# Kernel tuning notes

Measured on AMD Instinct MI355X. Metric: run time of the kernel, lower is better.

The kernel has to match this reference:

```python
import jax, jax.numpy as jnp
from jax import lax
import numpy as np

B, T, D = 64, 1024, 512
H = D // 2  # per-direction LSTM hidden size; concat fwd+bwd -> D


def _lstm_dir(x_tbd, W_ih, W_hh, b):
    # x_tbd: [T, B, D]; torch gate order i, f, g, o
    Bd = x_tbd.shape[1]
    Hd = W_hh.shape[1]

    def step(carry, x_t):
        h, c = carry
        g = x_t @ W_ih.T + h @ W_hh.T + b  # [B, 4H]
        i, f, gg, o = jnp.split(g, 4, axis=-1)
        c = jax.nn.sigmoid(f) * c + jax.nn.sigmoid(i) * jnp.tanh(gg)
        h = jax.nn.sigmoid(o) * jnp.tanh(c)
        return (h, c), h

    init = (jnp.zeros((Bd, Hd), x_tbd.dtype), jnp.zeros((Bd, Hd), x_tbd.dtype))
    _, hs = lax.scan(step, init, x_tbd)
    return hs  # [T, B, H]


def setup_inputs() -> dict:
    key = jax.random.key(0)
    ks = jax.random.split(key, 10)
    s_ih = 1.0 / np.sqrt(D)
    s_hh = 1.0 / np.sqrt(H)
    inp = {
        "x": jax.random.normal(ks[0], (B, T, D), jnp.float32),
        "W_ih_f": jax.random.uniform(ks[1], (4 * H, D), jnp.float32, -s_ih, s_ih),
        "W_hh_f": jax.random.uniform(ks[2], (4 * H, H), jnp.float32, -s_hh, s_hh),
        "b_f": jax.random.uniform(ks[3], (4 * H,), jnp.float32, -s_hh, s_hh),
        "W_ih_b": jax.random.uniform(ks[4], (4 * H, D), jnp.float32, -s_ih, s_ih),
        "W_hh_b": jax.random.uniform(ks[5], (4 * H, H), jnp.float32, -s_hh, s_hh),
        "b_b": jax.random.uniform(ks[6], (4 * H,), jnp.float32, -s_hh, s_hh),
        "lin_w": jax.random.normal(ks[7], (1, D), jnp.float32) * (1.0 / np.sqrt(D)),
        "lin_b": jnp.zeros((1,), jnp.float32),
        "ln_g": jnp.ones((D,), jnp.float32),
        "ln_b": jnp.zeros((D,), jnp.float32),
        "mask": jnp.ones((B, 1, T), dtype=bool),
        "input_len": T,
        "k": 20,
    }
    return inp


def reference(x, W_ih_f, W_hh_f, b_f, W_ih_b, W_hh_b, b_b, lin_w, lin_b,
              ln_g, ln_b, mask, input_len, k):
    x_tbd = jnp.transpose(x, (1, 0, 2))  # [T, B, D]
    h_f = _lstm_dir(x_tbd, W_ih_f, W_hh_f, b_f)                      # [T, B, H]
    h_b = _lstm_dir(x_tbd[::-1], W_ih_b, W_hh_b, b_b)[::-1]          # [T, B, H]
    lstm_o = jnp.transpose(jnp.concatenate([h_f, h_b], axis=-1), (1, 0, 2))  # [B, T, D]

    # linear -> squeeze -> softmax over seq dim
    logits = (lstm_o @ lin_w.T).squeeze(-1) + lin_b[0]  # [B, T]
    list_out = jax.nn.softmax(logits, axis=-1)

    # topk smallest (largest=False)
    _, indices = lax.top_k(-list_out, k)  # [B, k]

    # layer norm (eps=1e-5)
    mu = jnp.mean(lstm_o, axis=-1, keepdims=True)
    var = jnp.mean(jnp.square(lstm_o - mu), axis=-1, keepdims=True)
    lstm_o_n = (lstm_o - mu) * lax.rsqrt(var + 1e-5) * ln_g + ln_b

    # vectorized per-batch column scatter: mask[b, :, indices[b]] = False
    hit = jnp.zeros((B, T), dtype=bool).at[jnp.arange(B)[:, None], indices].set(True)
    sgn_mask = mask & ~hit[:, None, :]  # [B, 1, T]

    return (indices, lstm_o_n, sgn_mask)
```

## Files before the change

### kernel.cpp

```cpp
#include <hip/hip_runtime.h>
#include <math.h>

#define Bz 64
#define Tz 1024
#define Dz 512
#define Hz 256
#define Gz 1024
#define Kz 20

__device__ __forceinline__ float sigf(float x) { return 1.0f / (1.0f + __expf(-x)); }

__global__ __launch_bounds__(256) void init_ws(int* p) {
    int i = blockIdx.x * 256 + threadIdx.x;
    if (i < 100352) p[i] = 0;
}

__global__ __launch_bounds__(256) void gates_gemm(
    const float* __restrict__ x,
    const float* __restrict__ Wf, const float* __restrict__ Wb,
    const float* __restrict__ bf, const float* __restrict__ bb,
    float* __restrict__ G, int Tc, int base)
{
    __shared__ __align__(16) float As[16][68];
    __shared__ __align__(16) float Bs[16][68];
    const int tid   = threadIdx.x;
    const int mtile = blockIdx.x;
    const int sl    = blockIdx.y;
    const int dir   = blockIdx.z;

    const float* W    = dir ? Wb : Wf;
    const float* bias = dir ? bb : bf;
    const int s = base + sl;
    const int t = dir ? (Tz - 1 - s) : s;

    const int lr = tid >> 2;
    const int lk = (tid & 3) * 4;
    const float* Arow = W + (size_t)(mtile * 64 + lr) * Dz;
    const float* Brow = x + ((size_t)lr * Tz + t) * Dz;

    const int mg = tid >> 4;
    const int ng = tid & 15;
    float acc[4][4] = {};

    for (int kt = 0; kt < Dz; kt += 16) {
        float4 a4 = *(const float4*)(Arow + kt + lk);
        float4 b4 = *(const float4*)(Brow + kt + lk);
        __syncthreads();
        As[lk + 0][lr] = a4.x; As[lk + 1][lr] = a4.y;
        As[lk + 2][lr] = a4.z; As[lk + 3][lr] = a4.w;
        Bs[lk + 0][lr] = b4.x; Bs[lk + 1][lr] = b4.y;
        Bs[lk + 2][lr] = b4.z; Bs[lk + 3][lr] = b4.w;
        __syncthreads();
#pragma unroll
        for (int kk = 0; kk < 16; ++kk) {
            float4 av = *(const float4*)&As[kk][mg * 4];
            float4 bv = *(const float4*)&Bs[kk][ng * 4];
            acc[0][0] = fmaf(av.x, bv.x, acc[0][0]);
            acc[0][1] = fmaf(av.x, bv.y, acc[0][1]);
            acc[0][2] = fmaf(av.x, bv.z, acc[0][2]);
            acc[0][3] = fmaf(av.x, bv.w, acc[0][3]);
            acc[1][0] = fmaf(av.y, bv.x, acc[1][0]);
            acc[1][1] = fmaf(av.y, bv.y, acc[1][1]);
            acc[1][2] = fmaf(av.y, bv.z, acc[1][2]);
            acc[1][3] = fmaf(av.y, bv.w, acc[1][3]);
            acc[2][0] = fmaf(av.z, bv.x, acc[2][0]);
            acc[2][1] = fmaf(av.z, bv.y, acc[2][1]);
            acc[2][2] = fmaf(av.z, bv.z, acc[2][2]);
            acc[2][3] = fmaf(av.z, bv.w, acc[2][3]);
            acc[3][0] = fmaf(av.w, bv.x, acc[3][0]);
            acc[3][1] = fmaf(av.w, bv.y, acc[3][1]);
            acc[3][2] = fmaf(av.w, bv.z, acc[3][2]);
            acc[3][3] = fmaf(av.w, bv.w, acc[3][3]);
        }
    }
#pragma unroll
    for (int i = 0; i < 4; ++i) {
        int row = mtile * 64 + mg * 4 + i;
        float bvs = bias[row];
        float4 o;
        o.x = acc[i][0] + bvs; o.y = acc[i][1] + bvs;
        o.z = acc[i][2] + bvs; o.w = acc[i][3] + bvs;
        *(float4*)(G + (((size_t)dir * Gz + row) * Tc + sl) * 64 + ng * 4) = o;
    }
}

__global__ __launch_bounds__(512, 1) void lstm_rec(
    const float* __restrict__ G,
    const float* __restrict__ Whf, const float* __restrict__ Whb,
    float* __restrict__ hbuf,
    float* __restrict__ cbuf,
    float* __restrict__ out1,
    int* pflag, int Tc, int base)
{
    __shared__ __align__(16) float h_l[Hz * 64 + 512];
    __shared__ __align__(16) float part_l[4][16][64];

    const int tid = threadIdx.x;
    const int dir = blockIdx.x >> 6;
    const int g   = blockIdx.x & 63;
    const float* __restrict__ Whh = dir ? Whb : Whf;

    const int b    = tid & 63;
    const int w_id = __builtin_amdgcn_readfirstlane(tid >> 6);
    const int kq   = w_id & 3;
    const int rh   = w_id >> 2;

    const float* Wr[8];
#pragma unroll
    for (int i = 0; i < 8; ++i) {
        int rl = rh * 8 + i;
        int q = rl >> 2, j = rl & 3;
        Wr[i] = Whh + (size_t)(q * Hz + g * 4 + j) * Hz + kq * 64;
    }

    const int j_ = tid >> 6;
    float c_reg = 0.0f;
    if (tid < 256) c_reg = cbuf[((size_t)dir * Hz + g * 4 + j_) * 64 + b];

    for (int sl = 0; sl < Tc; ++sl) {
        const int s = base + sl;

        float gpre[4];
        if (tid < 256) {
#pragma unroll
            for (int q = 0; q < 4; ++q)
                gpre[q] = G[(((size_t)dir * Gz + q * Hz + g * 4 + j_) * Tc + sl) * 64 + b];
        }

        if (s > 0) {
            if (tid < 64) {
                const int* fp = pflag + dir * 64 + tid;
                for (;;) {
                    int v = __hip_atomic_load(fp, __ATOMIC_RELAXED,
                                              __HIP_MEMORY_SCOPE_AGENT);
                    if (__all(v >= s)) break;
                    __builtin_amdgcn_s_sleep(2);
                }
            }
            __syncthreads();
        }

        const unsigned long long* hsrc = (const unsigned long long*)
            (hbuf + (size_t)((s & 1) * 2 + dir) * Hz * 64);
        unsigned long long tmp[16];
#pragma unroll
        for (int jj = 0; jj < 16; ++jj)
            tmp[jj] = __hip_atomic_load(hsrc + jj * 512 + tid,
                                        __ATOMIC_RELAXED, __HIP_MEMORY_SCOPE_AGENT);
#pragma unroll
        for (int jj = 0; jj < 16; ++jj)
            ((unsigned long long*)h_l)[jj * 512 + tid] = tmp[jj];
        __syncthreads();

        float acc[8] = {};
        const float* hb = h_l + (size_t)(kq * 64) * 64 + b;
#pragma unroll 4
        for (int k = 0; k < 64; k += 4) {
            const float h0 = hb[(k + 0) * 64];
            const float h1 = hb[(k + 1) * 64];
            const float h2 = hb[(k + 2) * 64];
            const float h3 = hb[(k + 3) * 64];
#pragma unroll
            for (int i = 0; i < 8; ++i) {
                const float4 wv = *(const float4*)(Wr[i] + k);
                acc[i] = fmaf(h3, wv.w, fmaf(h2, wv.z,
                         fmaf(h1, wv.y, fmaf(h0, wv.x, acc[i]))));
            }
        }
#pragma unroll
        for (int i = 0; i < 8; ++i) part_l[kq][rh * 8 + i][b] = acc[i];
        __syncthreads();

        float hv = 0.0f;
        if (tid < 256) {
            float gv[4];
#pragma unroll
            for (int q = 0; q < 4; ++q) {
                const int rl = q * 4 + j_;
                gv[q] = gpre[q] + part_l[0][rl][b] + part_l[1][rl][b]
                      + part_l[2][rl][b] + part_l[3][rl][b];
            }
            const float gi = sigf(gv[0]);
            const float gf = sigf(gv[1]);
            const float gg = tanhf(gv[2]);
            const float go = sigf(gv[3]);
            c_reg = gf * c_reg + gi * gg;
            hv = go * tanhf(c_reg);
            const int hx = g * 4 + j_;
            __hip_atomic_store(
                hbuf + ((size_t)(((s + 1) & 1) * 2 + dir) * Hz + hx) * 64 + b, hv,
                __ATOMIC_RELAXED, __HIP_MEMORY_SCOPE_AGENT);
        }

        asm volatile("s_waitcnt vmcnt(0)" ::: "memory");
        __syncthreads();
        if (tid == 0)
            __hip_atomic_store(pflag + dir * 64 + g, s + 1,
                               __ATOMIC_RELAXED, __HIP_MEMORY_SCOPE_AGENT);

        if (tid < 256) {
            const int tt = dir ? (Tz - 1 - s) : s;
            out1[((size_t)b * Tz + tt) * Dz + dir * Hz + g * 4 + j_] = hv;
        }
    }
    if (tid < 256) cbuf[((size_t)dir * Hz + g * 4 + j_) * 64 + b] = c_reg;
}

__global__ __launch_bounds__(256) void head_kernel(
    const float* __restrict__ out1, const float* __restrict__ lin_w,
    const float* __restrict__ lin_b, const unsigned char* __restrict__ mask8,
    float* __restrict__ out0, float* __restrict__ out2)
{
    __shared__ __align__(16) float lw[Dz];
    __shared__ float llog[Tz];
    __shared__ unsigned char hit[Tz];
    __shared__ float redv[4];
    __shared__ int   redi[4];

    const int tid = threadIdx.x;
    const int bb  = blockIdx.x;
    for (int i = tid; i < Dz; i += 256) lw[i] = lin_w[i];
    for (int i = tid; i < Tz; i += 256) hit[i] = 0;
    __syncthreads();

    const int w = tid >> 6, lane = tid & 63;
    const float lbv = lin_b[0];
    for (int t = w; t < Tz; t += 4) {
        const float* rp = out1 + ((size_t)bb * Tz + t) * Dz + lane * 8;
        float4 a0 = *(const float4*)rp;
        float4 a1 = *(const float4*)(rp + 4);
        const float* wp = lw + lane * 8;
        float ps = a0.x * wp[0] + a0.y * wp[1] + a0.z * wp[2] + a0.w * wp[3]
                 + a1.x * wp[4] + a1.y * wp[5] + a1.z * wp[6] + a1.w * wp[7];
        for (int o = 32; o; o >>= 1) ps += __shfl_down(ps, o);
        if (lane == 0) llog[t] = ps + lbv;
    }
    __syncthreads();

    for (int it = 0; it < Kz; ++it) {
        float bv = 3.4e38f; int bi = Tz - 1;
        for (int t = tid; t < Tz; t += 256) {
            float v = llog[t];
            if (v < bv) { bv = v; bi = t; }
        }
        for (int o = 32; o; o >>= 1) {
            float ov = __shfl_down(bv, o);
            int   oi = __shfl_down(bi, o);
            if (ov < bv || (ov == bv && oi < bi)) { bv = ov; bi = oi; }
        }
        if (lane == 0) { redv[w] = bv; redi[w] = bi; }
        __syncthreads();
        if (tid == 0) {
            for (int qq = 1; qq < 4; ++qq)
                if (redv[qq] < bv || (redv[qq] == bv && redi[qq] < bi)) { bv = redv[qq]; bi = redi[qq]; }
            out0[bb * Kz + it] = (float)bi;
            llog[bi] = 3.4e38f;
            hit[bi] = 1;
        }
        __syncthreads();
    }
    for (int t = tid; t < Tz; t += 256) {
        bool mv = mask8[(size_t)bb * Tz + t] != 0;
        out2[(size_t)bb * Tz + t] = (mv && !hit[t]) ? 1.0f : 0.0f;
    }
}

__global__ __launch_bounds__(256) void ln_kernel(
    float* __restrict__ out1, const float* __restrict__ ln_g,
    const float* __restrict__ ln_b)
{
    const int tid = threadIdx.x;
    const int w = tid >> 6, lane = tid & 63;
    const size_t row = (size_t)blockIdx.x * 4 + w;
    float* rp = out1 + row * Dz + lane * 8;
    float4 a0 = *(float4*)rp;
    float4 a1 = *(float4*)(rp + 4);
    float s  = a0.x + a0.y + a0.z + a0.w + a1.x + a1.y + a1.z + a1.w;
    float sq = a0.x*a0.x + a0.y*a0.y + a0.z*a0.z + a0.w*a0.w
             + a1.x*a1.x + a1.y*a1.y + a1.z*a1.z + a1.w*a1.w;
    for (int o = 32; o; o >>= 1) { s += __shfl_down(s, o); sq += __shfl_down(sq, o); }
    s  = __shfl(s, 0);
    sq = __shfl(sq, 0);
    const float mu  = s * (1.0f / Dz);
    const float var = sq * (1.0f / Dz) - mu * mu;
    const float rs  = rsqrtf(var + 1e-5f);
    const float* gp = ln_g + lane * 8;
    const float* bp = ln_b + lane * 8;
    a0.x = (a0.x - mu) * rs * gp[0] + bp[0];
    a0.y = (a0.y - mu) * rs * gp[1] + bp[1];
    a0.z = (a0.z - mu) * rs * gp[2] + bp[2];
    a0.w = (a0.w - mu) * rs * gp[3] + bp[3];
    a1.x = (a1.x - mu) * rs * gp[4] + bp[4];
    a1.y = (a1.y - mu) * rs * gp[5] + bp[5];
    a1.z = (a1.z - mu) * rs * gp[6] + bp[6];
    a1.w = (a1.w - mu) * rs * gp[7] + bp[7];
    *(float4*)rp = a0;
    *(float4*)(rp + 4) = a1;
}

extern "C" void kernel_launch(void* const* d_in, const int* in_sizes, int n_in,
                              void* d_out, int out_size, void* d_ws, size_t ws_size,
                              hipStream_t stream)
{
    (void)in_sizes; (void)n_in; (void)out_size;
    const float* x     = (const float*)d_in[0];
    const float* Wif   = (const float*)d_in[1];
    const float* Whf   = (const float*)d_in[2];
    const float* bf    = (const float*)d_in[3];
    const float* Wib   = (const float*)d_in[4];
    const float* Whb   = (const float*)d_in[5];
    const float* bb    = (const float*)d_in[6];
    const float* lin_w = (const float*)d_in[7];
    const float* lin_b = (const float*)d_in[8];
    const float* ln_g  = (const float*)d_in[9];
    const float* ln_b  = (const float*)d_in[10];
    const unsigned char* mask8 = (const unsigned char*)d_in[11];

    float* ws    = (float*)d_ws;
    int*   flags = (int*)d_ws;
    float* hbuf  = ws + 2048;
    float* cbuf  = ws + 2048 + 65536;
    float* gates = ws + 2048 + 65536 + 32768;

    const size_t fixedBytes = (size_t)(2048 + 65536 + 32768) * 4;
    const size_t avail = ws_size > fixedBytes ? ws_size - fixedBytes : 0;
    int Tc = 8;
    for (int cand = 1024; cand >= 8; cand >>= 1) {
        if ((size_t)cand * (2ull * Gz * 64 * 4) <= avail) { Tc = cand; break; }
    }

    float* out0 = (float*)d_out;
    float* out1 = out0 + (size_t)Bz * Kz;
    float* out2 = out1 + (size_t)Bz * Tz * Dz;

    init_ws<<<dim3((100352 + 255) / 256), 256, 0, stream>>>((int*)d_ws);

    const int nChunks = Tz / Tc;
    for (int c = 0; c < nChunks; ++c) {
        const int base = c * Tc;
        gates_gemm<<<dim3(16, Tc, 2), 256, 0, stream>>>(x, Wif, Wib, bf, bb, gates, Tc, base);
        lstm_rec<<<dim3(128), 512, 0, stream>>>(gates, Whf, Whb, hbuf, cbuf, out1, flags, Tc, base);
    }
    head_kernel<<<dim3(Bz), 256, 0, stream>>>(out1, lin_w, lin_b, mask8, out0, out2);
    ln_kernel<<<dim3((Bz * Tz) / 4), 256, 0, stream>>>(out1, ln_g, ln_b);
}
```

Baseline: 12.51 ms.

## Repartition LSTM recurrence by batch slices with register-resident weights and stamped exchange

The recurrent kernel is reorganized so each of 256 blocks owns a 2-sample batch slice and a quarter of the hidden dimension. Its slice of W_hh is held in registers, which removes the per-step weight reload. Partial gate sums go to the other three quarter-blocks through a global buffer of stamped 64-bit value+step pairs. Each block polls those stamps, so the global per-step flag barrier and the full h broadcast through global memory are gone. The costs are much higher register pressure (128 weight floats per thread), a larger zeroed workspace, and a requirement that all 256 blocks be co-resident to avoid deadlock.

```diff
diff --git a/kernel.cpp b/kernel.cpp
--- a/kernel.cpp
+++ b/kernel.cpp
@@ -7,12 +7,19 @@
 #define Hz 256
 #define Gz 1024
 #define Kz 20
+#define NBS 32
+
+#define WS_ZERO_DWORDS (2097152 + 32768 + 32768)
 
 __device__ __forceinline__ float sigf(float x) { return 1.0f / (1.0f + __expf(-x)); }
+
+__device__ __forceinline__ unsigned long long packsv(float v, unsigned st) {
+    return ((unsigned long long)st << 32) | (unsigned long long)__float_as_uint(v);
+}
 
 __global__ __launch_bounds__(256) void init_ws(int* p) {
     int i = blockIdx.x * 256 + threadIdx.x;
-    if (i < 100352) p[i] = 0;
+    if (i < WS_ZERO_DWORDS) p[i] = 0;
 }
 
 __global__ __launch_bounds__(256) void gates_gemm(
@@ -87,123 +94,152 @@
 __global__ __launch_bounds__(512, 1) void lstm_rec(
     const float* __restrict__ G,
     const float* __restrict__ Whf, const float* __restrict__ Whb,
-    float* __restrict__ hbuf,
-    float* __restrict__ cbuf,
+    unsigned long long* __restrict__ xbuf,
+    float* __restrict__ hstate,
+    float* __restrict__ cstate,
     float* __restrict__ out1,
-    int* pflag, int Tc, int base)
-{
-    __shared__ __align__(16) float h_l[Hz * 64 + 512];
-    __shared__ __align__(16) float part_l[4][16][64];
+    int Tc, int base)
+{
+    __shared__ __align__(16) float h_l[64][2];
+    __shared__ __align__(16) float selfP[256][2];
+    __shared__ __align__(16) float gl[256][2];
 
     const int tid = threadIdx.x;
-    const int dir = blockIdx.x >> 6;
-    const int g   = blockIdx.x & 63;
+    const int blk = blockIdx.x;
+    const int dir = blk >> 7;
+    const int kq  = (blk >> 5) & 3;
+    const int bs  = blk & 31;
     const float* __restrict__ Whh = dir ? Whb : Whf;
 
-    const int b    = tid & 63;
-    const int w_id = __builtin_amdgcn_readfirstlane(tid >> 6);
-    const int kq   = w_id & 3;
-    const int rh   = w_id >> 2;
-
-    const float* Wr[8];
-#pragma unroll
-    for (int i = 0; i < 8; ++i) {
-        int rl = rh * 8 + i;
-        int q = rl >> 2, j = rl & 3;
-        Wr[i] = Whh + (size_t)(q * Hz + g * 4 + j) * Hz + kq * 64;
-    }
-
-    const int j_ = tid >> 6;
+    const int r0 = tid * 2;
+    float w0[64], w1[64];
+    {
+        const float* p0 = Whh + (size_t)r0 * Hz + kq * 64;
+        const float* p1 = p0 + Hz;
+#pragma unroll
+        for (int i = 0; i < 16; ++i) {
+            float4 a = *(const float4*)(p0 + 4 * i);
+            float4 c = *(const float4*)(p1 + 4 * i);
+            w0[4*i+0] = a.x; w0[4*i+1] = a.y; w0[4*i+2] = a.z; w0[4*i+3] = a.w;
+            w1[4*i+0] = c.x; w1[4*i+1] = c.y; w1[4*i+2] = c.z; w1[4*i+3] = c.w;
+        }
+    }
+    const int dst  = (tid >> 5) & 3;
+    const int rowp = (r0 >> 8) * 64 + (r0 & 63);
+
+    const int arow = tid >> 1;
+    const int ab   = tid & 1;
+    const int growA = (arow >> 6) * 256 + kq * 64 + (arow & 63);
+    const int bglo  = bs * 2;
+
+    int srcs[3];
+    { int n = 0; for (int ss = 0; ss < 4; ++ss) if (ss != kq) srcs[n++] = ss; }
+
+    size_t ob[2], ib[2];
+#pragma unroll
+    for (int p = 0; p < 2; ++p) {
+        ob[p] = (((((size_t)p*2 + dir)*NBS + bs)*4 + dst)*4 + kq)*512 + (size_t)rowp*2;
+        ib[p] = ((((size_t)p*2 + dir)*NBS + bs)*4 + kq)*4*512 + (size_t)arow*2 + ab;
+    }
+
     float c_reg = 0.0f;
-    if (tid < 256) c_reg = cbuf[((size_t)dir * Hz + g * 4 + j_) * 64 + b];
+    {
+        const size_t sb = ((size_t)(dir * NBS + bs) * 4 + kq) * 128;
+        if (tid < 128) {
+            h_l[tid >> 1][tid & 1] = hstate[sb + tid];
+            c_reg = cstate[sb + tid];
+        }
+    }
+    __syncthreads();
 
     for (int sl = 0; sl < Tc; ++sl) {
         const int s = base + sl;
-
-        float gpre[4];
-        if (tid < 256) {
-#pragma unroll
-            for (int q = 0; q < 4; ++q)
-                gpre[q] = G[(((size_t)dir * Gz + q * Hz + g * 4 + j_) * Tc + sl) * 64 + b];
-        }
-
-        if (s > 0) {
-            if (tid < 64) {
-                const int* fp = pflag + dir * 64 + tid;
-                for (;;) {
-                    int v = __hip_atomic_load(fp, __ATOMIC_RELAXED,
-                                              __HIP_MEMORY_SCOPE_AGENT);
-                    if (__all(v >= s)) break;
-                    __builtin_amdgcn_s_sleep(2);
-                }
+        const unsigned stamp = (unsigned)(s + 1);
+        const int par = s & 1;
+
+        const float gval =
+            G[(((size_t)dir * Gz + growA) * Tc + sl) * 64 + (bglo + ab)];
+
+        float a00 = 0.f, a01 = 0.f, a10 = 0.f, a11 = 0.f;
+#pragma unroll
+        for (int kk = 0; kk < 64; kk += 2) {
+            const float4 hv = *(const float4*)(&h_l[kk][0]);
+            a00 = fmaf(w0[kk],     hv.x, a00);
+            a01 = fmaf(w0[kk],     hv.y, a01);
+            a10 = fmaf(w1[kk],     hv.x, a10);
+            a11 = fmaf(w1[kk],     hv.y, a11);
+            a00 = fmaf(w0[kk + 1], hv.z, a00);
+            a01 = fmaf(w0[kk + 1], hv.w, a01);
+            a10 = fmaf(w1[kk + 1], hv.z, a10);
+            a11 = fmaf(w1[kk + 1], hv.w, a11);
+        }
+
+        if (dst == kq) {
+            *(float4*)&selfP[rowp][0] = make_float4(a00, a01, a10, a11);
+        } else {
+            unsigned long long* op = xbuf + ob[par];
+            __hip_atomic_store(op + 0, packsv(a00, stamp),
+                               __ATOMIC_RELAXED, __HIP_MEMORY_SCOPE_AGENT);
+            __hip_atomic_store(op + 1, packsv(a01, stamp),
+                               __ATOMIC_RELAXED, __HIP_MEMORY_SCOPE_AGENT);
+            __hip_atomic_store(op + 2, packsv(a10, stamp),
+                               __ATOMIC_RELAXED, __HIP_MEMORY_SCOPE_AGENT);
+            __hip_atomic_store(op + 3, packsv(a11, stamp),
+                               __ATOMIC_RELAXED, __HIP_MEMORY_SCOPE_AGENT);
+        }
+        __syncthreads();
+
+        {
+            const unsigned long long* ibp = xbuf + ib[par];
+            const unsigned long long* i0 = ibp + (size_t)srcs[0] * 512;
+            const unsigned long long* i1 = ibp + (size_t)srcs[1] * 512;
+            const unsigned long long* i2 = ibp + (size_t)srcs[2] * 512;
+            unsigned long long v0 = __hip_atomic_load(i0, __ATOMIC_RELAXED,
+                                                      __HIP_MEMORY_SCOPE_AGENT);
+            unsigned long long v1 = __hip_atomic_load(i1, __ATOMIC_RELAXED,
+                                                      __HIP_MEMORY_SCOPE_AGENT);
+            unsigned long long v2 = __hip_atomic_load(i2, __ATOMIC_RELAXED,
+                                                      __HIP_MEMORY_SCOPE_AGENT);
+            for (;;) {
+                const bool o0 = (unsigned)(v0 >> 32) == stamp;
+                const bool o1 = (unsigned)(v1 >> 32) == stamp;
+                const bool o2 = (unsigned)(v2 >> 32) == stamp;
+                if (o0 & o1 & o2) break;
+                __builtin_amdgcn_s_sleep(1);
+                if (!o0) v0 = __hip_atomic_load(i0, __ATOMIC_RELAXED,
+                                                __HIP_MEMORY_SCOPE_AGENT);
+                if (!o1) v1 = __hip_atomic_load(i1, __ATOMIC_RELAXED,
+                                                __HIP_MEMORY_SCOPE_AGENT);
+                if (!o2) v2 = __hip_atomic_load(i2, __ATOMIC_RELAXED,
+                                                __HIP_MEMORY_SCOPE_AGENT);
             }
-            __syncthreads();
-        }
-
-        const unsigned long long* hsrc = (const unsigned long long*)
-            (hbuf + (size_t)((s & 1) * 2 + dir) * Hz * 64);
-        unsigned long long tmp[16];
-#pragma unroll
-        for (int jj = 0; jj < 16; ++jj)
-            tmp[jj] = __hip_atomic_load(hsrc + jj * 512 + tid,
-                                        __ATOMIC_RELAXED, __HIP_MEMORY_SCOPE_AGENT);
-#pragma unroll
-        for (int jj = 0; jj < 16; ++jj)
-            ((unsigned long long*)h_l)[jj * 512 + tid] = tmp[jj];
-        __syncthreads();
-
-        float acc[8] = {};
-        const float* hb = h_l + (size_t)(kq * 64) * 64 + b;
-#pragma unroll 4
-        for (int k = 0; k < 64; k += 4) {
-            const float h0 = hb[(k + 0) * 64];
-            const float h1 = hb[(k + 1) * 64];
-            const float h2 = hb[(k + 2) * 64];
-            const float h3 = hb[(k + 3) * 64];
-#pragma unroll
-            for (int i = 0; i < 8; ++i) {
-                const float4 wv = *(const float4*)(Wr[i] + k);
-                acc[i] = fmaf(h3, wv.w, fmaf(h2, wv.z,
-                         fmaf(h1, wv.y, fmaf(h0, wv.x, acc[i]))));
-            }
-        }
-#pragma unroll
-        for (int i = 0; i < 8; ++i) part_l[kq][rh * 8 + i][b] = acc[i];
-        __syncthreads();
-
-        float hv = 0.0f;
-        if (tid < 256) {
-            float gv[4];
-#pragma unroll
-            for (int q = 0; q < 4; ++q) {
-                const int rl = q * 4 + j_;
-                gv[q] = gpre[q] + part_l[0][rl][b] + part_l[1][rl][b]
-                      + part_l[2][rl][b] + part_l[3][rl][b];
-            }
-            const float gi = sigf(gv[0]);
-            const float gf = sigf(gv[1]);
-            const float gg = tanhf(gv[2]);
-            const float go = sigf(gv[3]);
+            gl[arow][ab] = gval + selfP[arow][ab]
+                         + __uint_as_float((unsigned)v0)
+                         + __uint_as_float((unsigned)v1)
+                         + __uint_as_float((unsigned)v2);
+        }
+        __syncthreads();
+
+        if (tid < 128) {
+            const int bj = tid >> 1, bb2 = tid & 1;
+            const float gi = sigf(gl[bj][bb2]);
+            const float gf = sigf(gl[64 + bj][bb2]);
+            const float gg = tanhf(gl[128 + bj][bb2]);
+            const float go = sigf(gl[192 + bj][bb2]);
             c_reg = gf * c_reg + gi * gg;
-            hv = go * tanhf(c_reg);
-            const int hx = g * 4 + j_;
-            __hip_atomic_store(
-                hbuf + ((size_t)(((s + 1) & 1) * 2 + dir) * Hz + hx) * 64 + b, hv,
-                __ATOMIC_RELAXED, __HIP_MEMORY_SCOPE_AGENT);
-        }
-
-        asm volatile("s_waitcnt vmcnt(0)" ::: "memory");
-        __syncthreads();
-        if (tid == 0)
-            __hip_atomic_store(pflag + dir * 64 + g, s + 1,
-                               __ATOMIC_RELAXED, __HIP_MEMORY_SCOPE_AGENT);
-
-        if (tid < 256) {
+            const float hv = go * tanhf(c_reg);
+            h_l[bj][bb2] = hv;
             const int tt = dir ? (Tz - 1 - s) : s;
-            out1[((size_t)b * Tz + tt) * Dz + dir * Hz + g * 4 + j_] = hv;
-        }
-    }
-    if (tid < 256) cbuf[((size_t)dir * Hz + g * 4 + j_) * 64 + b] = c_reg;
+            out1[((size_t)(bglo + bb2) * Tz + tt) * Dz + dir * Hz + kq * 64 + bj] = hv;
+        }
+        __syncthreads();
+    }
+
+    if (tid < 128) {
+        const size_t sb = ((size_t)(dir * NBS + bs) * 4 + kq) * 128;
+        hstate[sb + tid] = h_l[tid >> 1][tid & 1];
+        cstate[sb + tid] = c_reg;
+    }
 }
 
 __global__ __launch_bounds__(256) void head_kernel(
@@ -316,13 +352,13 @@
     const float* ln_b  = (const float*)d_in[10];
     const unsigned char* mask8 = (const unsigned char*)d_in[11];
 
-    float* ws    = (float*)d_ws;
-    int*   flags = (int*)d_ws;
-    float* hbuf  = ws + 2048;
-    float* cbuf  = ws + 2048 + 65536;
-    float* gates = ws + 2048 + 65536 + 32768;
-
-    const size_t fixedBytes = (size_t)(2048 + 65536 + 32768) * 4;
+    float* ws = (float*)d_ws;
+    unsigned long long* xbuf = (unsigned long long*)ws;
+    float* hstate = ws + 2097152;
+    float* cstate = hstate + 32768;
+    float* gates  = cstate + 32768;
+
+    const size_t fixedBytes = (size_t)(2097152 + 65536) * 4;
     const size_t avail = ws_size > fixedBytes ? ws_size - fixedBytes : 0;
     int Tc = 8;
     for (int cand = 1024; cand >= 8; cand >>= 1) {
@@ -333,13 +369,14 @@
     float* out1 = out0 + (size_t)Bz * Kz;
     float* out2 = out1 + (size_t)Bz * Tz * Dz;
 
-    init_ws<<<dim3((100352 + 255) / 256), 256, 0, stream>>>((int*)d_ws);
+    init_ws<<<dim3((WS_ZERO_DWORDS + 255) / 256), 256, 0, stream>>>((int*)d_ws);
 
     const int nChunks = Tz / Tc;
     for (int c = 0; c < nChunks; ++c) {
         const int base = c * Tc;
         gates_gemm<<<dim3(16, Tc, 2), 256, 0, stream>>>(x, Wif, Wib, bf, bb, gates, Tc, base);
-        lstm_rec<<<dim3(128), 512, 0, stream>>>(gates, Whf, Whb, hbuf, cbuf, out1, flags, Tc, base);
+        lstm_rec<<<dim3(256), 512, 0, stream>>>(gates, Whf, Whb, xbuf, hstate, cstate,
+                                                out1, Tc, base);
     }
     head_kernel<<<dim3(Bz), 256, 0, stream>>>(out1, lin_w, lin_b, mask8, out0, out2);
     ln_kernel<<<dim3((Bz * Tz) / 4), 256, 0, stream>>>(out1, ln_g, ln_b);
```

After: 10.51 ms. 16.0% less time.

## Fuse input-gate GEMM and recurrence into one persistent producer-consumer kernel

Applied to the files above, without the earlier changes.

Replaces the chunked gates_gemm plus lstm_rec launches with a single persistent kernel. 128 blocks run the recurrence, each owning a batch slice and a K-quarter with W_hh held in registers and partial sums exchanged through stamped global buffers. The other 128 blocks compute the input projection into an 8-slot ring and are gated by progress flags. This removes per-chunk launch overhead and the large gates buffer, and overlaps the input GEMM with the sequential recurrence. In exchange it depends on all 256 blocks being co-resident and on fine-grained spin synchronization across blocks, and the 128 registers per thread used to hold weights risk spilling.

```diff
diff --git a/kernel.cpp b/kernel.cpp
--- a/kernel.cpp
+++ b/kernel.cpp
@@ -8,202 +8,287 @@
 #define Gz 1024
 #define Kz 20
 
+#define CTRL_DW  256
+#define XBUF_U64 786432
+#define ZERO_DW  (CTRL_DW + XBUF_U64 * 2)
+#define RING_DW  (8 * 2 * 1024 * 64)
+
 __device__ __forceinline__ float sigf(float x) { return 1.0f / (1.0f + __expf(-x)); }
+
+__device__ __forceinline__ unsigned long long packsv(float v, unsigned st) {
+    return ((unsigned long long)st << 32) | (unsigned long long)__float_as_uint(v);
+}
+__device__ __forceinline__ unsigned long long pack2(float a, float b) {
+    return ((unsigned long long)__float_as_uint(b) << 32) |
+           (unsigned long long)__float_as_uint(a);
+}
 
 __global__ __launch_bounds__(256) void init_ws(int* p) {
     int i = blockIdx.x * 256 + threadIdx.x;
-    if (i < 100352) p[i] = 0;
-}
-
-__global__ __launch_bounds__(256) void gates_gemm(
+    if (i < ZERO_DW) p[i] = 0;
+}
+
+__global__ __launch_bounds__(512, 1) void fused_lstm(
     const float* __restrict__ x,
-    const float* __restrict__ Wf, const float* __restrict__ Wb,
-    const float* __restrict__ bf, const float* __restrict__ bb,
-    float* __restrict__ G, int Tc, int base)
+    const float* __restrict__ Wif, const float* __restrict__ Whf,
+    const float* __restrict__ bf,
+    const float* __restrict__ Wib, const float* __restrict__ Whb,
+    const float* __restrict__ bb,
+    float* __restrict__ out1, int* __restrict__ ctrl)
 {
-    __shared__ __align__(16) float As[16][68];
-    __shared__ __align__(16) float Bs[16][68];
-    const int tid   = threadIdx.x;
-    const int mtile = blockIdx.x;
-    const int sl    = blockIdx.y;
-    const int dir   = blockIdx.z;
-
-    const float* W    = dir ? Wb : Wf;
-    const float* bias = dir ? bb : bf;
-    const int s = base + sl;
-    const int t = dir ? (Tz - 1 - s) : s;
-
-    const int lr = tid >> 2;
-    const int lk = (tid & 3) * 4;
-    const float* Arow = W + (size_t)(mtile * 64 + lr) * Dz;
-    const float* Brow = x + ((size_t)lr * Tz + t) * Dz;
-
-    const int mg = tid >> 4;
-    const int ng = tid & 15;
-    float acc[4][4] = {};
-
-    for (int kt = 0; kt < Dz; kt += 16) {
-        float4 a4 = *(const float4*)(Arow + kt + lk);
-        float4 b4 = *(const float4*)(Brow + kt + lk);
+    __shared__ __align__(16) float smem[34880];
+    int* gcnt = ctrl;
+    int* prog = ctrl + 8;
+    unsigned long long* xbuf = (unsigned long long*)(ctrl + CTRL_DW);
+    float* Gring = (float*)(ctrl + CTRL_DW + XBUF_U64 * 2);
+
+    const int tid = threadIdx.x;
+    const int blk = blockIdx.x;
+
+    if (blk < 128) {
+        const int dir = blk >> 6;
+        const int kq  = (blk >> 4) & 3;
+        const int bs  = blk & 15;
+        const float* __restrict__ Whh = dir ? Whb : Whf;
+
+        float* h_l   = smem;
+        float* selfP = smem + 256;
+        float* gl    = smem + 1280;
+
+        const int r0 = tid * 2;
+        float w0[64], w1[64];
+        {
+            const float* p0 = Whh + (size_t)r0 * Hz + kq * 64;
+            const float* p1 = p0 + Hz;
+#pragma unroll
+            for (int i = 0; i < 16; ++i) {
+                float4 a = *(const float4*)(p0 + 4 * i);
+                float4 c = *(const float4*)(p1 + 4 * i);
+                w0[4*i+0]=a.x; w0[4*i+1]=a.y; w0[4*i+2]=a.z; w0[4*i+3]=a.w;
+                w1[4*i+0]=c.x; w1[4*i+1]=c.y; w1[4*i+2]=c.z; w1[4*i+3]=c.w;
+            }
+        }
+        const int dst  = (r0 >> 6) & 3;
+        const int rowp = (r0 >> 8) * 64 + (r0 & 63);
+        const int srci = kq - (kq > dst ? 1 : 0);
+
+        const int arow  = tid >> 1;
+        const int bp    = tid & 1;
+        const int growA = (arow >> 6) * 256 + kq * 64 + (arow & 63);
+        const int bglo  = bs * 4;
+
+        size_t ob[2], ib[2];
+#pragma unroll
+        for (int p = 0; p < 2; ++p) {
+            size_t o = ((((size_t)p * 2 + dir) * 16 + bs) * 4 + dst) * 3 + srci;
+            ob[p] = o * 1024 + (size_t)rowp * 4;
+            size_t q = ((((size_t)p * 2 + dir) * 16 + bs) * 4 + kq) * 3;
+            ib[p] = q * 1024 + (size_t)arow * 4 + 2 * bp;
+        }
+
+        for (int i = tid; i < 256; i += 512) h_l[i] = 0.0f;
+        float c_reg = 0.0f;
+        const int rr = tid >> 2, bb2 = tid & 3;
         __syncthreads();
-        As[lk + 0][lr] = a4.x; As[lk + 1][lr] = a4.y;
-        As[lk + 2][lr] = a4.z; As[lk + 3][lr] = a4.w;
-        Bs[lk + 0][lr] = b4.x; Bs[lk + 1][lr] = b4.y;
-        Bs[lk + 2][lr] = b4.z; Bs[lk + 3][lr] = b4.w;
+
+        for (int s = 0; s < Tz; ++s) {
+            const unsigned stamp = (unsigned)(s + 1);
+            const int par = s & 1;
+
+            if ((s & 1) == 0) {
+                const int sp = s >> 1;
+                const int tgt = ((sp >> 2) + 1) * 16;
+                if (tid < 64) {
+                    const int* gp = gcnt + dir * 4 + (sp & 3);
+                    while (__hip_atomic_load(gp, __ATOMIC_RELAXED,
+                                             __HIP_MEMORY_SCOPE_AGENT) < tgt)
+                        __builtin_amdgcn_s_sleep(2);
+                }
+                __syncthreads();
+            }
+
+            const unsigned long long* Gp = (const unsigned long long*)
+                (Gring + ((size_t)((s & 7) * 2 + dir) * 1024 + growA) * 64
+                       + bglo + 2 * bp);
+            unsigned long long gv = __hip_atomic_load(Gp, __ATOMIC_RELAXED,
+                                                      __HIP_MEMORY_SCOPE_AGENT);
+
+            float a0[4] = {}, a1[4] = {};
+#pragma unroll
+            for (int k = 0; k < 64; ++k) {
+                const float4 hv = *(const float4*)(h_l + k * 4);
+                const float wa = w0[k], wc = w1[k];
+                a0[0] = fmaf(wa, hv.x, a0[0]); a0[1] = fmaf(wa, hv.y, a0[1]);
+                a0[2] = fmaf(wa, hv.z, a0[2]); a0[3] = fmaf(wa, hv.w, a0[3]);
+                a1[0] = fmaf(wc, hv.x, a1[0]); a1[1] = fmaf(wc, hv.y, a1[1]);
+                a1[2] = fmaf(wc, hv.z, a1[2]); a1[3] = fmaf(wc, hv.w, a1[3]);
+            }
+
+            if (dst == kq) {
+                *(float4*)(selfP + rowp * 4)     = make_float4(a0[0],a0[1],a0[2],a0[3]);
+                *(float4*)(selfP + rowp * 4 + 4) = make_float4(a1[0],a1[1],a1[2],a1[3]);
+            } else {
+                unsigned long long* op = xbuf + ob[par];
+#pragma unroll
+                for (int j = 0; j < 4; ++j)
+                    __hip_atomic_store(op + j, packsv(a0[j], stamp),
+                                       __ATOMIC_RELAXED, __HIP_MEMORY_SCOPE_AGENT);
+#pragma unroll
+                for (int j = 0; j < 4; ++j)
+                    __hip_atomic_store(op + 4 + j, packsv(a1[j], stamp),
+                                       __ATOMIC_RELAXED, __HIP_MEMORY_SCOPE_AGENT);
+            }
+            __syncthreads();
+
+            {
+                const unsigned long long* i0 = xbuf + ib[par];
+                const unsigned long long* ps[6] =
+                    { i0, i0 + 1, i0 + 1024, i0 + 1025, i0 + 2048, i0 + 2049 };
+                unsigned long long v[6];
+#pragma unroll
+                for (int j = 0; j < 6; ++j)
+                    v[j] = __hip_atomic_load(ps[j], __ATOMIC_RELAXED,
+                                             __HIP_MEMORY_SCOPE_AGENT);
+                for (;;) {
+                    bool ok = true;
+#pragma unroll
+                    for (int j = 0; j < 6; ++j)
+                        ok &= ((unsigned)(v[j] >> 32) == stamp);
+                    if (ok) break;
+                    __builtin_amdgcn_s_sleep(1);
+#pragma unroll
+                    for (int j = 0; j < 6; ++j)
+                        if ((unsigned)(v[j] >> 32) != stamp)
+                            v[j] = __hip_atomic_load(ps[j], __ATOMIC_RELAXED,
+                                                     __HIP_MEMORY_SCOPE_AGENT);
+                }
+                gl[arow * 4 + 2 * bp] =
+                    __uint_as_float((unsigned)gv) + selfP[arow * 4 + 2 * bp]
+                    + __uint_as_float((unsigned)v[0])
+                    + __uint_as_float((unsigned)v[2])
+                    + __uint_as_float((unsigned)v[4]);
+                gl[arow * 4 + 2 * bp + 1] =
+                    __uint_as_float((unsigned)(gv >> 32)) + selfP[arow * 4 + 2 * bp + 1]
+                    + __uint_as_float((unsigned)v[1])
+                    + __uint_as_float((unsigned)v[3])
+                    + __uint_as_float((unsigned)v[5]);
+            }
+            __syncthreads();
+
+            float hv_s = 0.0f;
+            if (tid < 256) {
+                const float gi = sigf(gl[rr * 4 + bb2]);
+                const float gf = sigf(gl[(64 + rr) * 4 + bb2]);
+                const float gg = tanhf(gl[(128 + rr) * 4 + bb2]);
+                const float go = sigf(gl[(192 + rr) * 4 + bb2]);
+                c_reg = gf * c_reg + gi * gg;
+                hv_s = go * tanhf(c_reg);
+                h_l[rr * 4 + bb2] = hv_s;
+            }
+            __syncthreads();
+            if (kq == 0 && tid == 0)
+                __hip_atomic_store(prog + dir * 16 + bs, s,
+                                   __ATOMIC_RELAXED, __HIP_MEMORY_SCOPE_AGENT);
+            if (tid < 256) {
+                const int tt = dir ? (Tz - 1 - s) : s;
+                out1[((size_t)(bglo + bb2) * Tz + tt) * Dz + dir * Hz + kq * 64 + rr] = hv_s;
+            }
+        }
+    } else {
+        const int g2      = blk - 128;
+        const int rowtile = g2 & 15;
+        const int dir     = (g2 >> 4) & 1;
+        const int phase   = (g2 >> 5) & 3;
+        const float* __restrict__ Wih  = dir ? Wib : Wif;
+        const float* __restrict__ bias = dir ? bb : bf;
+
+        float* Bs  = smem;
+        float* A_l = smem + 2112;
+
+        const int mg = tid >> 5;
+        const int ng = tid & 31;
+        const float4 bias4 = *(const float4*)(bias + rowtile * 64 + mg * 4);
+
+        for (int idx = tid * 4; idx < 64 * 512; idx += 2048) {
+            const int r = idx >> 9, k = idx & 511;
+            const float4 a = *(const float4*)(Wih + (size_t)(rowtile * 64 + r) * Dz + k);
+            A_l[(k + 0) * 64 + r] = a.x; A_l[(k + 1) * 64 + r] = a.y;
+            A_l[(k + 2) * 64 + r] = a.z; A_l[(k + 3) * 64 + r] = a.w;
+        }
         __syncthreads();
-#pragma unroll
-        for (int kk = 0; kk < 16; ++kk) {
-            float4 av = *(const float4*)&As[kk][mg * 4];
-            float4 bv = *(const float4*)&Bs[kk][ng * 4];
-            acc[0][0] = fmaf(av.x, bv.x, acc[0][0]);
-            acc[0][1] = fmaf(av.x, bv.y, acc[0][1]);
-            acc[0][2] = fmaf(av.x, bv.z, acc[0][2]);
-            acc[0][3] = fmaf(av.x, bv.w, acc[0][3]);
-            acc[1][0] = fmaf(av.y, bv.x, acc[1][0]);
-            acc[1][1] = fmaf(av.y, bv.y, acc[1][1]);
-            acc[1][2] = fmaf(av.y, bv.z, acc[1][2]);
-            acc[1][3] = fmaf(av.y, bv.w, acc[1][3]);
-            acc[2][0] = fmaf(av.z, bv.x, acc[2][0]);
-            acc[2][1] = fmaf(av.z, bv.y, acc[2][1]);
-            acc[2][2] = fmaf(av.z, bv.z, acc[2][2]);
-            acc[2][3] = fmaf(av.z, bv.w, acc[2][3]);
-            acc[3][0] = fmaf(av.w, bv.x, acc[3][0]);
-            acc[3][1] = fmaf(av.w, bv.y, acc[3][1]);
-            acc[3][2] = fmaf(av.w, bv.z, acc[3][2]);
-            acc[3][3] = fmaf(av.w, bv.w, acc[3][3]);
+
+        const int nn   = tid & 127;
+        const int ko   = (tid >> 7) * 4;
+        const int bcol = nn & 63;
+        const int slx  = nn >> 6;
+        const int ssl  = ng >> 4;
+        const int bc0  = (ng & 15) * 4;
+
+        for (int sp = phase; sp < 512; sp += 4) {
+            const int s0 = 2 * sp;
+            const int ttx = dir ? (Tz - 1 - (s0 + slx)) : (s0 + slx);
+            const float* xp = x + ((size_t)bcol * Tz + ttx) * Dz;
+
+            float4 bq = *(const float4*)(xp + ko);
+            float acc[4][4] = {};
+            for (int kt = 0; kt < 512; kt += 16) {
+                __syncthreads();
+                Bs[(ko + 0) * 132 + nn] = bq.x;
+                Bs[(ko + 1) * 132 + nn] = bq.y;
+                Bs[(ko + 2) * 132 + nn] = bq.z;
+                Bs[(ko + 3) * 132 + nn] = bq.w;
+                __syncthreads();
+                if (kt + 16 < 512) bq = *(const float4*)(xp + kt + 16 + ko);
+#pragma unroll
+                for (int kk = 0; kk < 16; ++kk) {
+                    const float4 av = *(const float4*)(A_l + (kt + kk) * 64 + mg * 4);
+                    const float4 bv = *(const float4*)(Bs + kk * 132 + ng * 4);
+                    acc[0][0]=fmaf(av.x,bv.x,acc[0][0]); acc[0][1]=fmaf(av.x,bv.y,acc[0][1]);
+                    acc[0][2]=fmaf(av.x,bv.z,acc[0][2]); acc[0][3]=fmaf(av.x,bv.w,acc[0][3]);
+                    acc[1][0]=fmaf(av.y,bv.x,acc[1][0]); acc[1][1]=fmaf(av.y,bv.y,acc[1][1]);
+                    acc[1][2]=fmaf(av.y,bv.z,acc[1][2]); acc[1][3]=fmaf(av.y,bv.w,acc[1][3]);
+                    acc[2][0]=fmaf(av.z,bv.x,acc[2][0]); acc[2][1]=fmaf(av.z,bv.y,acc[2][1]);
+                    acc[2][2]=fmaf(av.z,bv.z,acc[2][2]); acc[2][3]=fmaf(av.z,bv.w,acc[2][3]);
+                    acc[3][0]=fmaf(av.w,bv.x,acc[3][0]); acc[3][1]=fmaf(av.w,bv.y,acc[3][1]);
+                    acc[3][2]=fmaf(av.w,bv.z,acc[3][2]); acc[3][3]=fmaf(av.w,bv.w,acc[3][3]);
+                }
+            }
+
+            if (sp >= 4) {
+                const int tgt = 2 * sp - 6;
+                if (tid < 64) {
+                    for (;;) {
+                        int pv = (tid < 16)
+                            ? __hip_atomic_load(prog + dir * 16 + tid,
+                                                __ATOMIC_RELAXED, __HIP_MEMORY_SCOPE_AGENT)
+                            : 0x7fffffff;
+                        if (__all(pv >= tgt)) break;
+                        __builtin_amdgcn_s_sleep(2);
+                    }
+                }
+            }
+            __syncthreads();
+
+            const int slot = (s0 + ssl) & 7;
+            float* gbase = Gring + ((size_t)(slot * 2 + dir) * 1024
+                                    + rowtile * 64 + mg * 4) * 64 + bc0;
+#pragma unroll
+            for (int i = 0; i < 4; ++i) {
+                const float bv4 = (i == 0) ? bias4.x : (i == 1) ? bias4.y
+                                 : (i == 2) ? bias4.z : bias4.w;
+                unsigned long long* gp = (unsigned long long*)(gbase + (size_t)i * 64);
+                __hip_atomic_store(gp,     pack2(acc[i][0] + bv4, acc[i][1] + bv4),
+                                   __ATOMIC_RELAXED, __HIP_MEMORY_SCOPE_AGENT);
+                __hip_atomic_store(gp + 1, pack2(acc[i][2] + bv4, acc[i][3] + bv4),
+                                   __ATOMIC_RELAXED, __HIP_MEMORY_SCOPE_AGENT);
+            }
+            asm volatile("s_waitcnt vmcnt(0)" ::: "memory");
+            __syncthreads();
+            if (tid == 0)
+                __hip_atomic_fetch_add(gcnt + dir * 4 + (sp & 3), 1,
+                                       __ATOMIC_RELAXED, __HIP_MEMORY_SCOPE_AGENT);
         }
     }
-#pragma unroll
-    for (int i = 0; i < 4; ++i) {
-        int row = mtile * 64 + mg * 4 + i;
-        float bvs = bias[row];
-        float4 o;
-        o.x = acc[i][0] + bvs; o.y = acc[i][1] + bvs;
-        o.z = acc[i][2] + bvs; o.w = acc[i][3] + bvs;
-        *(float4*)(G + (((size_t)dir * Gz + row) * Tc + sl) * 64 + ng * 4) = o;
-    }
-}
-
-__global__ __launch_bounds__(512, 1) void lstm_rec(
-    const float* __restrict__ G,
-    const float* __restrict__ Whf, const float* __restrict__ Whb,
-    float* __restrict__ hbuf,
-    float* __restrict__ cbuf,
-    float* __restrict__ out1,
-    int* pflag, int Tc, int base)
-{
-    __shared__ __align__(16) float h_l[Hz * 64 + 512];
-    __shared__ __align__(16) float part_l[4][16][64];
-
-    const int tid = threadIdx.x;
-    const int dir = blockIdx.x >> 6;
-    const int g   = blockIdx.x & 63;
-    const float* __restrict__ Whh = dir ? Whb : Whf;
-
-    const int b    = tid & 63;
-    const int w_id = __builtin_amdgcn_readfirstlane(tid >> 6);
-    const int kq   = w_id & 3;
-    const int rh   = w_id >> 2;
-
-    const float* Wr[8];
-#pragma unroll
-    for (int i = 0; i < 8; ++i) {
-        int rl = rh * 8 + i;
-        int q = rl >> 2, j = rl & 3;
-        Wr[i] = Whh + (size_t)(q * Hz + g * 4 + j) * Hz + kq * 64;
-    }
-
-    const int j_ = tid >> 6;
-    float c_reg = 0.0f;
-    if (tid < 256) c_reg = cbuf[((size_t)dir * Hz + g * 4 + j_) * 64 + b];
-
-    for (int sl = 0; sl < Tc; ++sl) {
-        const int s = base + sl;
-
-        float gpre[4];
-        if (tid < 256) {
-#pragma unroll
-            for (int q = 0; q < 4; ++q)
-                gpre[q] = G[(((size_t)dir * Gz + q * Hz + g * 4 + j_) * Tc + sl) * 64 + b];
-        }
-
-        if (s > 0) {
-            if (tid < 64) {
-                const int* fp = pflag + dir * 64 + tid;
-                for (;;) {
-                    int v = __hip_atomic_load(fp, __ATOMIC_RELAXED,
-                                              __HIP_MEMORY_SCOPE_AGENT);
-                    if (__all(v >= s)) break;
-                    __builtin_amdgcn_s_sleep(2);
-                }
-            }
-            __syncthreads();
-        }
-
-        const unsigned long long* hsrc = (const unsigned long long*)
-            (hbuf + (size_t)((s & 1) * 2 + dir) * Hz * 64);
-        unsigned long long tmp[16];
-#pragma unroll
-        for (int jj = 0; jj < 16; ++jj)
-            tmp[jj] = __hip_atomic_load(hsrc + jj * 512 + tid,
-                                        __ATOMIC_RELAXED, __HIP_MEMORY_SCOPE_AGENT);
-#pragma unroll
-        for (int jj = 0; jj < 16; ++jj)
-            ((unsigned long long*)h_l)[jj * 512 + tid] = tmp[jj];
-        __syncthreads();
-
-        float acc[8] = {};
-        const float* hb = h_l + (size_t)(kq * 64) * 64 + b;
-#pragma unroll 4
-        for (int k = 0; k < 64; k += 4) {
-            const float h0 = hb[(k + 0) * 64];
-            const float h1 = hb[(k + 1) * 64];
-            const float h2 = hb[(k + 2) * 64];
-            const float h3 = hb[(k + 3) * 64];
-#pragma unroll
-            for (int i = 0; i < 8; ++i) {
-                const float4 wv = *(const float4*)(Wr[i] + k);
-                acc[i] = fmaf(h3, wv.w, fmaf(h2, wv.z,
-                         fmaf(h1, wv.y, fmaf(h0, wv.x, acc[i]))));
-            }
-        }
-#pragma unroll
-        for (int i = 0; i < 8; ++i) part_l[kq][rh * 8 + i][b] = acc[i];
-        __syncthreads();
-
-        float hv = 0.0f;
-        if (tid < 256) {
-            float gv[4];
-#pragma unroll
-            for (int q = 0; q < 4; ++q) {
-                const int rl = q * 4 + j_;
-                gv[q] = gpre[q] + part_l[0][rl][b] + part_l[1][rl][b]
-                      + part_l[2][rl][b] + part_l[3][rl][b];
-            }
-            const float gi = sigf(gv[0]);
-            const float gf = sigf(gv[1]);
-            const float gg = tanhf(gv[2]);
-            const float go = sigf(gv[3]);
-            c_reg = gf * c_reg + gi * gg;
-            hv = go * tanhf(c_reg);
-            const int hx = g * 4 + j_;
-            __hip_atomic_store(
-                hbuf + ((size_t)(((s + 1) & 1) * 2 + dir) * Hz + hx) * 64 + b, hv,
-                __ATOMIC_RELAXED, __HIP_MEMORY_SCOPE_AGENT);
-        }
-
-        asm volatile("s_waitcnt vmcnt(0)" ::: "memory");
-        __syncthreads();
-        if (tid == 0)
-            __hip_atomic_store(pflag + dir * 64 + g, s + 1,
-                               __ATOMIC_RELAXED, __HIP_MEMORY_SCOPE_AGENT);
-
-        if (tid < 256) {
-            const int tt = dir ? (Tz - 1 - s) : s;
-            out1[((size_t)b * Tz + tt) * Dz + dir * Hz + g * 4 + j_] = hv;
-        }
-    }
-    if (tid < 256) cbuf[((size_t)dir * Hz + g * 4 + j_) * 64 + b] = c_reg;
 }
 
 __global__ __launch_bounds__(256) void head_kernel(
@@ -302,7 +387,7 @@
                               void* d_out, int out_size, void* d_ws, size_t ws_size,
                               hipStream_t stream)
 {
-    (void)in_sizes; (void)n_in; (void)out_size;
+    (void)in_sizes; (void)n_in; (void)out_size; (void)ws_size;
     const float* x     = (const float*)d_in[0];
     const float* Wif   = (const float*)d_in[1];
     const float* Whf   = (const float*)d_in[2];
@@ -316,31 +401,15 @@
     const float* ln_b  = (const float*)d_in[10];
     const unsigned char* mask8 = (const unsigned char*)d_in[11];
 
-    float* ws    = (float*)d_ws;
-    int*   flags = (int*)d_ws;
-    float* hbuf  = ws + 2048;
-    float* cbuf  = ws + 2048 + 65536;
-    float* gates = ws + 2048 + 65536 + 32768;
-
-    const size_t fixedBytes = (size_t)(2048 + 65536 + 32768) * 4;
-    const size_t avail = ws_size > fixedBytes ? ws_size - fixedBytes : 0;
-    int Tc = 8;
-    for (int cand = 1024; cand >= 8; cand >>= 1) {
-        if ((size_t)cand * (2ull * Gz * 64 * 4) <= avail) { Tc = cand; break; }
-    }
+    int* ctrl = (int*)d_ws;
 
     float* out0 = (float*)d_out;
     float* out1 = out0 + (size_t)Bz * Kz;
     float* out2 = out1 + (size_t)Bz * Tz * Dz;
 
-    init_ws<<<dim3((100352 + 255) / 256), 256, 0, stream>>>((int*)d_ws);
-
-    const int nChunks = Tz / Tc;
-    for (int c = 0; c < nChunks; ++c) {
-        const int base = c * Tc;
-        gates_gemm<<<dim3(16, Tc, 2), 256, 0, stream>>>(x, Wif, Wib, bf, bb, gates, Tc, base);
-        lstm_rec<<<dim3(128), 512, 0, stream>>>(gates, Whf, Whb, hbuf, cbuf, out1, flags, Tc, base);
-    }
+    init_ws<<<dim3((ZERO_DW + 255) / 256), 256, 0, stream>>>(ctrl);
+    fused_lstm<<<dim3(256), 512, 0, stream>>>(x, Wif, Whf, bf, Wib, Whb, bb,
+                                              out1, ctrl);
     head_kernel<<<dim3(Bz), 256, 0, stream>>>(out1, lin_w, lin_b, mask8, out0, out2);
     ln_kernel<<<dim3((Bz * Tz) / 4), 256, 0, stream>>>(out1, ln_g, ln_b);
 }
```

New measurement: 13.34 ms. 1.07x slower.
